# Optimization experiments

Hardware: AMD Instinct MI355X
Metric: run time of the kernel (lower is better)

## Reference

```python
import jax, jax.numpy as jnp
import numpy as np

N, E, F, H, R, NB, G, C = 100000, 500000, 128, 64, 16, 30, 1000, 10


def setup_inputs() -> dict:
    key = jax.random.key(0)
    ks = jax.random.split(key, 12)
    s = 0.05
    x = jax.random.normal(ks[0], (N, F), jnp.float32)
    edge_index = jax.random.randint(ks[1], (2, E), 0, N, dtype=jnp.int32)
    edge_norm = jax.random.uniform(ks[2], (E,), jnp.float32)
    edge_type = jax.random.randint(ks[3], (E,), 0, R, dtype=jnp.int32)
    seq_lengths = jnp.full((G,), N // G, dtype=jnp.int32)  # 1000 graphs x 100 nodes
    return dict(
        x=x, edge_index=edge_index, edge_norm=edge_norm, edge_type=edge_type,
        seq_lengths=seq_lengths, avec=0,
        w1_rel=jax.random.normal(ks[4], (F, H), jnp.float32) * s,
        w1_root=jax.random.normal(ks[5], (F, H), jnp.float32) * s,
        b1=jnp.zeros((H,), jnp.float32),
        bases=jax.random.normal(ks[6], (NB, H, H), jnp.float32) * s,
        comp=jax.random.normal(ks[7], (R, NB), jnp.float32) * s,
        w2_root=jax.random.normal(ks[8], (H, H), jnp.float32) * s,
        b2=jnp.zeros((H,), jnp.float32),
        lin_w=jax.random.normal(ks[9], (2 * (F + H), H), jnp.float32) * s,
        lin_b=jnp.zeros((H,), jnp.float32),
        fc_w=jax.random.normal(ks[10], (H, C), jnp.float32) * s,
        fc_b=jnp.zeros((C,), jnp.float32),
    )


def reference(x, edge_index, edge_norm, edge_type, seq_lengths, avec,
              w1_rel, w1_root, b1, bases, comp, w2_root, b2,
              lin_w, lin_b, fc_w, fc_b):
    src, dst = edge_index[0], edge_index[1]

    # --- GraphConv (PyG): out_i = W_rel @ sum_{j->i} w_ji x_j + W_root x_i + b
    msg = x[src] * edge_norm[:, None]                       # [E, F]
    agg = jax.ops.segment_sum(msg, dst, num_segments=N)     # [N, F]
    h = agg @ w1_rel + x @ w1_root + b1                     # [N, H]

    # --- RGCNConv with basis decomposition, mean aggregation per relation
    W = jnp.einsum('rb,bio->rio', comp, bases)              # [R, H, H]
    hs = h[src]                                             # [E, H]
    out = h @ w2_root + b2                                  # root transform + bias
    for r in range(R):  # small fixed relation count
        m = (edge_type == r).astype(h.dtype)                # [E]
        s_r = jax.ops.segment_sum(hs * m[:, None], dst, num_segments=N)
        c_r = jax.ops.segment_sum(m, dst, num_segments=N)
        out = out + (s_r / jnp.maximum(c_r, 1.0)[:, None]) @ W[r]

    feats = jnp.concatenate([x, out], axis=-1)              # [N, F+H]

    # --- ragged per-graph sum & max pooling (replaces the Python loop)
    bounds = jnp.cumsum(seq_lengths)
    gid = jnp.searchsorted(bounds, jnp.arange(N), side='right')  # [N] graph ids
    gsum = jax.ops.segment_sum(feats, gid, num_segments=G)       # [G, F+H]
    gmax = jax.ops.segment_max(feats, gid, num_segments=G)       # [G, F+H]

    hidden = jax.nn.relu(jnp.concatenate([gsum, gmax], -1) @ lin_w + lin_b)
    # dropout is identity at inference
    logits = hidden @ fc_w + fc_b                           # [G, C]
    if avec:
        return logits
    return jax.nn.log_softmax(logits, -1)
```

## Files before the change

### kernel.cpp

```cpp
#include <hip/hip_runtime.h>
#include <hip/hip_bf16.h>

#define NN 100000
#define NE 500000
#define FD 128
#define HD 64
#define RR 16
#define NBASE 30
#define GG 1000
#define CC 10
#define NGROUP 6250
#define NBLK ((NE + 255) / 256)
#define NDBLK ((NN + 256) / 256)
#define NOBLK (NN / 16)
#define NPBLK ((NGROUP + 3) / 4)
#define TOTZ (NN * RR)
#define ZBLK ((TOTZ + 1023) / 1024)


typedef __attribute__((ext_vector_type(8))) short bf16x8;
typedef __attribute__((ext_vector_type(4))) float f32x4;

__device__ inline unsigned short f2b(float x) {
  __hip_bfloat16 b = __float2bfloat16(x);
  return *reinterpret_cast<unsigned short*>(&b);
}
__device__ inline float b2f(unsigned short u) {
  return __uint_as_float(((unsigned)u) << 16);
}
__device__ inline unsigned pk2(float a, float b) {
  return (unsigned)f2b(a) | ((unsigned)f2b(b) << 16);
}

__device__ inline int block_scan_incl(int v, int* ps, int t) {
  ps[t] = v;
  __syncthreads();
  for (int off = 1; off < 256; off <<= 1) {
    int u = (t >= off) ? ps[t - off] : 0;
    __syncthreads();
    ps[t] += u;
    __syncthreads();
  }
  return ps[t];
}

__global__ void k_prep(const float* comp, const float* bases, const float* w_root,
                       const float* w_rel, const float* w2, const int* seq,
                       unsigned short* Wt, unsigned short* wcat2, unsigned short* w2t,
                       int* zbase, int* bounds) {
  int bx = blockIdx.x;
  if (bx < 256) {
    int idx = bx * 256 + threadIdx.x;
    int r = idx >> 12, kj = idx & 4095;
    int k = kj >> 6, n = kj & 63;
    float acc = 0.0f;
    for (int b = 0; b < NBASE; ++b)
      acc += comp[r * NBASE + b] * bases[b * 4096 + kj];
    int sk = (k & 15) * 4 + (k >> 4);
    Wt[(r << 12) + n * 64 + sk] = f2b(acc);
  } else if (bx < 336) {
    int idx = (bx - 256) * 256 + threadIdx.x;
    if (idx < 16384) {
      int n = idx >> 7, k = idx & 127;
      float v = (n < 64) ? w_root[k * 64 + n] : w_rel[k * 64 + (n - 64)];
      int nt = n >> 4, m = n & 15;
      int s = k >> 5, q = (k >> 3) & 3, j = k & 7;
      wcat2[(((nt * 4 + s) * 64) + q * 16 + m) * 8 + j] = f2b(v);
    } else if (idx < 16384 + 4096) {
      int i2 = idx - 16384;
      int n = i2 >> 6, k = i2 & 63;
      int sk = (k & 15) * 4 + (k >> 4);
      w2t[n * 64 + sk] = f2b(w2[k * 64 + n]);
    }
  } else if (bx == 336) {
    __shared__ int ps[256];
    int t = threadIdx.x;
    int loc[4];
    int ss = 0;
    if (t < 250) {
      for (int i = 0; i < 4; ++i) { loc[i] = seq[t * 4 + i]; ss += loc[i]; }
    }
    int incl = block_scan_incl(ss, ps, t);
    int base = incl - ss;
    if (t < 250) {
      int run = base;
      for (int i = 0; i < 4; ++i) { run += loc[i]; bounds[t * 4 + i] = run; }
    }
  } else {
    int idx = (bx - 337) * 1024 + threadIdx.x * 4;
    if (idx < TOTZ)
      *reinterpret_cast<int4*>(zbase + idx) = make_int4(0, 0, 0, 0);
  }
}

__global__ __launch_bounds__(256) void k_projhists(
    const float* x, const unsigned short* wcat2, const float* b1,
    unsigned short* hroot_bf, unsigned short* xw_bf,
    const int* ei, const int* etype, int* bch, int* hist2) {
  __shared__ unsigned short wsh[16384];
  __shared__ int lh[RR];
  if (blockIdx.x < NBLK) {
    if (threadIdx.x < RR) lh[threadIdx.x] = 0;
    __syncthreads();
    int e = blockIdx.x * 256 + threadIdx.x;
    if (e < NE) {
      int t = etype[e];
      atomicAdd(&lh[t], 1);
      atomicAdd(&hist2[ei[NE + e] * RR + t], 1);
    }
    __syncthreads();
    if (threadIdx.x < RR) bch[blockIdx.x * RR + threadIdx.x] = lh[threadIdx.x];
    return;
  }
  int bx = blockIdx.x - NBLK;
  int wv = threadIdx.x >> 6, l = threadIdx.x & 63, m = l & 15, q = l >> 4;
  int g = bx * 4 + wv;
  bool active = (g < NGROUP);
  int gc = active ? g : (NGROUP - 1);
  size_t n0 = (size_t)gc * 16;
  const float* xr = x + (n0 + m) * FD + q * 8;
  float4 xv[8];
#pragma unroll
  for (int s = 0; s < 4; ++s) {
    xv[2 * s] = *reinterpret_cast<const float4*>(xr + s * 32);
    xv[2 * s + 1] = *reinterpret_cast<const float4*>(xr + s * 32 + 4);
  }
  {
    const uint4* wsrc = reinterpret_cast<const uint4*>(wcat2);
    uint4* wdst = reinterpret_cast<uint4*>(wsh);
#pragma unroll
    for (int r = 0; r < 8; ++r)
      wdst[r * 256 + threadIdx.x] = wsrc[r * 256 + threadIdx.x];
  }
  __syncthreads();
  if (!active) return;
  bf16x8 afr[4];
#pragma unroll
  for (int s = 0; s < 4; ++s) {
    float4 xa = xv[2 * s], xb = xv[2 * s + 1];
    bf16x8 a;
    a[0] = (short)f2b(xa.x); a[1] = (short)f2b(xa.y);
    a[2] = (short)f2b(xa.z); a[3] = (short)f2b(xa.w);
    a[4] = (short)f2b(xb.x); a[5] = (short)f2b(xb.y);
    a[6] = (short)f2b(xb.z); a[7] = (short)f2b(xb.w);
    afr[s] = a;
  }
  f32x4 acc[8];
#pragma unroll
  for (int nt = 0; nt < 8; ++nt) acc[nt] = (f32x4){0, 0, 0, 0};
#pragma unroll
  for (int s = 0; s < 4; ++s) {
#pragma unroll
    for (int nt = 0; nt < 8; ++nt) {
      bf16x8 b = *reinterpret_cast<const bf16x8*>(wsh + (size_t)((nt * 4 + s) * 64 + l) * 8);
      acc[nt] = __builtin_amdgcn_mfma_f32_16x16x32_bf16(afr[s], b, acc[nt], 0, 0, 0);
    }
  }
  float bv[4];
#pragma unroll
  for (int nt = 0; nt < 4; ++nt) bv[nt] = b1[nt * 16 + m];
#pragma unroll
  for (int i = 0; i < 4; ++i) {
    size_t row = (n0 + q * 4 + i) * 64 + m * 4;
    uint2 oh, ox;
    oh.x = pk2(acc[0][i] + bv[0], acc[1][i] + bv[1]);
    oh.y = pk2(acc[2][i] + bv[2], acc[3][i] + bv[3]);
    ox.x = pk2(acc[4][i], acc[5][i]);
    ox.y = pk2(acc[6][i], acc[7][i]);
    *reinterpret_cast<uint2*>(hroot_bf + row) = oh;
    *reinterpret_cast<uint2*>(xw_bf + row) = ox;
  }
}

__device__ inline int dst_degree(const int* hist2, int dst) {
  const int4* hp = reinterpret_cast<const int4*>(hist2 + dst * RR);
  int4 a = hp[0], b = hp[1], c = hp[2], d = hp[3];
  return a.x + a.y + a.z + a.w + b.x + b.y + b.z + b.w +
         c.x + c.y + c.z + c.w + d.x + d.y + d.z + d.w;
}

__global__ void k_scanA(const int* hist2, int* bsum) {
  __shared__ int red[256];
  int t = threadIdx.x;
  int dst = blockIdx.x * 256 + t;
  red[t] = (dst < NN) ? dst_degree(hist2, dst) : 0;
  __syncthreads();
  for (int s = 128; s; s >>= 1) {
    if (t < s) red[t] += red[t + s];
    __syncthreads();
  }
  if (t == 0) bsum[blockIdx.x] = red[0];
}

__global__ void k_scanC(const int* hist2, const int* bsum, int* rowptr_d, int* ctr_d) {
  int t = threadIdx.x;
  int dst = blockIdx.x * 256 + t;
  int v = (dst < NN) ? dst_degree(hist2, dst) : 0;
  __shared__ int ps[256];
  int incl = block_scan_incl(v, ps, t);
  int ex = bsum[blockIdx.x] + incl - v;
  if (dst <= NN) { rowptr_d[dst] = ex; ctr_d[dst] = ex; }
}

__global__ void k_bscan(const int* bch, int* bsum, int* bbase, int* offs) {
  __shared__ int part[16][17], chunkbase[16][17];
  __shared__ int colbase[16];
  __shared__ int ps[256];
  int t = threadIdx.x;
  {
    int i0 = t * 2, i1 = t * 2 + 1;
    int l0 = (i0 < NDBLK) ? bsum[i0] : 0;
    int l1 = (i1 < NDBLK) ? bsum[i1] : 0;
    int sa = l0 + l1;
    int incla = block_scan_incl(sa, ps, t);
    int run = incla - sa;
    if (i0 < NDBLK) bsum[i0] = run;
    run += l0;
    if (i1 < NDBLK) bsum[i1] = run;
  }
  __syncthreads();
  int ty = t & 15, ck = t >> 4;
  const int CH = (NBLK + 15) / 16;
  int b0 = ck * CH, b1 = min(b0 + CH, NBLK);
  int s = 0;
  for (int b = b0; b < b1; ++b) s += bch[b * 16 + ty];
  part[ck][ty] = s;
  __syncthreads();
  if (t < 16) {
    int run = 0;
    for (int c = 0; c < 16; ++c) { chunkbase[c][t] = run; run += part[c][t]; }
    colbase[t] = run;
  }
  __syncthreads();
  if (t == 0) {
    int run = 0;
    for (int r = 0; r < RR; ++r) { int v = colbase[r]; offs[r] = run; colbase[r] = run; run += v; }
    offs[RR] = run;
  }
  __syncthreads();
  {
    int run = colbase[ty] + chunkbase[ck][ty];
    for (int b = b0; b < b1; ++b) {
      int v = bch[b * 16 + ty];
      bbase[b * 16 + ty] = run;
      run += v;
    }
  }
}

__global__ void k_sort(const int* ei, const int* etype, const float* enorm,
                       const int* bbase, const int* hist2, int* ctr_d,
                       uint4* tse, uint2* esen) {
  __shared__ int lcnt[RR];
  if (threadIdx.x < RR) lcnt[threadIdx.x] = 0;
  __syncthreads();
  int e = blockIdx.x * 256 + threadIdx.x;
  if (e >= NE) return;
  int t = etype[e];
  int rank = atomicAdd(&lcnt[t], 1);
  int p = bbase[blockIdx.x * RR + t] + rank;
  int src = ei[e];
  int dst = ei[NE + e];
  int cnt = hist2[dst * RR + t];
  float inv = 1.0f / (float)max(cnt, 1);
  int pos = atomicAdd(&ctr_d[dst], 1);
  esen[pos] = make_uint2((unsigned)src, __float_as_uint(enorm[e]));
  tse[p] = make_uint4((unsigned)src, __float_as_uint(inv), (unsigned)pos, 0u);
}

__global__ __launch_bounds__(256) void k_gconv_seg(const int* rowptr_d, const uint2* esen,
    const unsigned short* xw_bf, const unsigned short* hroot_bf, unsigned short* h_bf) {
  int wv = threadIdx.x >> 6, l = threadIdx.x & 63;
  int c4 = l & 15, eq = l >> 4;
  int dst = blockIdx.x * 4 + wv;
  int lo = rowptr_d[dst];
  int hi = rowptr_d[dst + 1];
  float4 acc = {0.0f, 0.0f, 0.0f, 0.0f};
  for (int base0 = lo; base0 < hi; base0 += 64) {
    int n = min(64, hi - base0);
    int sv = 0;
    float nv = 0.0f;
    if (l < n) {
      uint2 se = esen[base0 + l];
      sv = (int)se.x;
      nv = __uint_as_float(se.y);
    }
    int k4max = (n + 3) >> 2;
    for (int k4 = 0; k4 < k4max; ++k4) {
      int eid = k4 * 4 + eq;
      int s = __shfl(sv, eid);
      float w = __shfl(nv, eid);
      if (eid < n) {
        uint2 v = *reinterpret_cast<const uint2*>(xw_bf + (size_t)s * 64 + c4 * 4);
        acc.x += b2f((unsigned short)(v.x & 0xffffu)) * w;
        acc.y += b2f((unsigned short)(v.x >> 16)) * w;
        acc.z += b2f((unsigned short)(v.y & 0xffffu)) * w;
        acc.w += b2f((unsigned short)(v.y >> 16)) * w;
      }
    }
  }
  acc.x += __shfl_xor(acc.x, 16); acc.y += __shfl_xor(acc.y, 16);
  acc.z += __shfl_xor(acc.z, 16); acc.w += __shfl_xor(acc.w, 16);
  acc.x += __shfl_xor(acc.x, 32); acc.y += __shfl_xor(acc.y, 32);
  acc.z += __shfl_xor(acc.z, 32); acc.w += __shfl_xor(acc.w, 32);
  if (l < 16) {
    uint2 hb = *reinterpret_cast<const uint2*>(hroot_bf + (size_t)dst * 64 + l * 4);
    acc.x += b2f((unsigned short)(hb.x & 0xffffu));
    acc.y += b2f((unsigned short)(hb.x >> 16));
    acc.z += b2f((unsigned short)(hb.y & 0xffffu));
    acc.w += b2f((unsigned short)(hb.y >> 16));
    uint2 o;
    o.x = pk2(acc.x, acc.y);
    o.y = pk2(acc.z, acc.w);
    *reinterpret_cast<uint2*>(h_bf + (size_t)dst * 64 + l * 4) = o;
  }
}

__global__ __launch_bounds__(256) void k_rgcn_y(const uint4* tse, const int* offs,
    const unsigned short* h_bf, const unsigned short* Wt, unsigned short* y_bf) {
  int r = blockIdx.x;
  int lo = offs[r], hi = offs[r + 1];
  int cnt = hi - lo;
  int wv = threadIdx.x >> 6;
  int l = threadIdx.x & 63;
  int m = l & 15, q = l >> 4;
  int ngroups = (cnt + 15) / 16;
  const unsigned short* Wr = Wt + (r << 12);
  bf16x8 bfr[2][4];
#pragma unroll
  for (int s = 0; s < 2; ++s)
#pragma unroll
    for (int nt = 0; nt < 4; ++nt)
      bfr[s][nt] = *reinterpret_cast<const bf16x8*>(Wr + (nt * 16 + m) * 64 + s * 32 + q * 8);

  for (int g = blockIdx.y * 4 + wv; g < ngroups; g += gridDim.y * 4) {
    int base = lo + g * 16;
    int ne = min(16, hi - base);
    int p = base + ((m < ne) ? m : 0);
    uint4 t4 = tse[p];
    int src = (int)t4.x;
    float inv = __uint_as_float(t4.y);
    int pos = (int)t4.z;
    f32x4 acc[4];
#pragma unroll
    for (int nt = 0; nt < 4; ++nt) acc[nt] = (f32x4){0, 0, 0, 0};
    const unsigned short* hrow = h_bf + (size_t)src * 64 + q * 8;
#pragma unroll
    for (int s = 0; s < 2; ++s) {
      bf16x8 afr = *reinterpret_cast<const bf16x8*>(hrow + s * 32);
#pragma unroll
      for (int nt = 0; nt < 4; ++nt)
        acc[nt] = __builtin_amdgcn_mfma_f32_16x16x32_bf16(afr, bfr[s][nt], acc[nt], 0, 0, 0);
    }
#pragma unroll
    for (int i = 0; i < 4; ++i) {
      int row = q * 4 + i;
      float ir = __shfl(inv, row);
      int pr = __shfl(pos, row);
      if (row < ne) {
        uint2 o;
        o.x = pk2(acc[0][i] * ir, acc[1][i] * ir);
        o.y = pk2(acc[2][i] * ir, acc[3][i] * ir);
        *reinterpret_cast<uint2*>(y_bf + (size_t)pr * 64 + m * 4) = o;
      }
    }
  }
}

__global__ __launch_bounds__(256) void k_out(const int* rowptr_d, const unsigned short* y_bf,
    const unsigned short* h_bf, const unsigned short* w2t, const float* b2,
    const int* bounds, float* psum_p, float* pmax_p) {
  __shared__ float ldsC[16][68];
  __shared__ int gidv[16];
  int wv = threadIdx.x >> 6, l = threadIdx.x & 63;
  int c4 = l & 15, eq = l >> 4;
  size_t d0 = (size_t)blockIdx.x * 16;
  if (threadIdx.x < 16) {
    int dst = (int)d0 + threadIdx.x;
    int lo2 = 0, hi2 = GG;
    while (lo2 < hi2) {
      int mid = (lo2 + hi2) >> 1;
      if (bounds[mid] <= dst) lo2 = mid + 1; else hi2 = mid;
    }
    gidv[threadIdx.x] = lo2;
  }
  for (int dd = 0; dd < 4; ++dd) {
    int dst = (int)d0 + wv * 4 + dd;
    int lo = rowptr_d[dst];
    int hi = rowptr_d[dst + 1];
    float4 acc = {0.0f, 0.0f, 0.0f, 0.0f};
    for (int row = lo + eq; row < hi; row += 4) {
      uint2 v = *reinterpret_cast<const uint2*>(y_bf + (size_t)row * 64 + c4 * 4);
      acc.x += b2f((unsigned short)(v.x & 0xffffu));
      acc.y += b2f((unsigned short)(v.x >> 16));
      acc.z += b2f((unsigned short)(v.y & 0xffffu));
      acc.w += b2f((unsigned short)(v.y >> 16));
    }
    acc.x += __shfl_xor(acc.x, 16); acc.y += __shfl_xor(acc.y, 16);
    acc.z += __shfl_xor(acc.z, 16); acc.w += __shfl_xor(acc.w, 16);
    acc.x += __shfl_xor(acc.x, 32); acc.y += __shfl_xor(acc.y, 32);
    acc.z += __shfl_xor(acc.z, 32); acc.w += __shfl_xor(acc.w, 32);
    if (l < 16)
      *reinterpret_cast<float4*>(&ldsC[wv * 4 + dd][l * 4]) = acc;
  }
  __syncthreads();
  int m = l & 15, q = l >> 4, nt = wv;
  float bb = b2[nt * 16 + m];
  f32x4 acc;
#pragma unroll
  for (int i = 0; i < 4; ++i) acc[i] = ldsC[q * 4 + i][m * 4 + nt] + bb;
#pragma unroll
  for (int s = 0; s < 2; ++s) {
    bf16x8 a = *reinterpret_cast<const bf16x8*>(h_bf + (d0 + m) * 64 + s * 32 + q * 8);
    bf16x8 b = *reinterpret_cast<const bf16x8*>(w2t + (nt * 16 + m) * 64 + s * 32 + q * 8);
    acc = __builtin_amdgcn_mfma_f32_16x16x32_bf16(a, b, acc, 0, 0, 0);
  }
  int c = nt * 16 + m;
  int gA = gidv[0];
  float sA = 0.0f, xA = -3.4e38f, sB = 0.0f, xB = -3.4e38f;
#pragma unroll
  for (int i = 0; i < 4; ++i) {
    int gi = gidv[q * 4 + i];
    if (gi == gA) { sA += acc[i]; xA = fmaxf(xA, acc[i]); }
    else          { sB += acc[i]; xB = fmaxf(xB, acc[i]); }
  }
#pragma unroll
  for (int off = 16; off <= 32; off <<= 1) {
    sA += __shfl_xor(sA, off); xA = fmaxf(xA, __shfl_xor(xA, off));
    sB += __shfl_xor(sB, off); xB = fmaxf(xB, __shfl_xor(xB, off));
  }
  if (q == 0) {
    size_t base = (size_t)blockIdx.x * 128;
    psum_p[base + c] = sA;
    psum_p[base + 64 + c] = sB;
    pmax_p[base + c] = xA;
    pmax_p[base + 64 + c] = xB;
  }
}

__global__ __launch_bounds__(256) void k_head(const float* x, const int* bounds,
    const float* psum_p, const float* pmax_p, const float* lin_w, const float* lin_b,
    const float* fc_w, const float* fc_b, float* dout) {
  __shared__ float4 psum[8][32], pmax[8][32];
  __shared__ float gsum[192], gmax[192];
  __shared__ float part[4][64];
  __shared__ float hid[HD], lg[CC], mred[2];
  int g = blockIdx.x, t = threadIdx.x;
  int lo = (g == 0) ? 0 : bounds[g - 1];
  int hi = bounds[g];
  int nn = hi - lo;
  {
    int c4 = t & 31, ch = t >> 5;
    int a = lo + (nn * ch) / 8, b = lo + (nn * (ch + 1)) / 8;
    float4 s = {0, 0, 0, 0};
    float4 mx = {-3.4e38f, -3.4e38f, -3.4e38f, -3.4e38f};
    const float* bp = x + (size_t)a * FD + c4 * 4;
    int n = a;
    for (; n + 4 <= b; n += 4) {
      float4 v0 = *reinterpret_cast<const float4*>(bp);
      float4 v1 = *reinterpret_cast<const float4*>(bp + FD);
      float4 v2 = *reinterpret_cast<const float4*>(bp + 2 * FD);
      float4 v3 = *reinterpret_cast<const float4*>(bp + 3 * FD);
      bp += 4 * FD;
      s.x += v0.x + v1.x + v2.x + v3.x;
      s.y += v0.y + v1.y + v2.y + v3.y;
      s.z += v0.z + v1.z + v2.z + v3.z;
      s.w += v0.w + v1.w + v2.w + v3.w;
      mx.x = fmaxf(fmaxf(fmaxf(mx.x, v0.x), fmaxf(v1.x, v2.x)), v3.x);
      mx.y = fmaxf(fmaxf(fmaxf(mx.y, v0.y), fmaxf(v1.y, v2.y)), v3.y);
      mx.z = fmaxf(fmaxf(fmaxf(mx.z, v0.z), fmaxf(v1.z, v2.z)), v3.z);
      mx.w = fmaxf(fmaxf(fmaxf(mx.w, v0.w), fmaxf(v1.w, v2.w)), v3.w);
    }
    for (; n < b; ++n) {
      float4 v = *reinterpret_cast<const float4*>(bp);
      bp += FD;
      s.x += v.x; s.y += v.y; s.z += v.z; s.w += v.w;
      mx.x = fmaxf(mx.x, v.x); mx.y = fmaxf(mx.y, v.y);
      mx.z = fmaxf(mx.z, v.z); mx.w = fmaxf(mx.w, v.w);
    }
    psum[ch][c4] = s;
    pmax[ch][c4] = mx;
  }
  __syncthreads();
  if (t < 32) {
    float4 s = psum[0][t], m = pmax[0][t];
#pragma unroll
    for (int ch = 1; ch < 8; ++ch) {
      float4 ps = psum[ch][t], pm = pmax[ch][t];
      s.x += ps.x; s.y += ps.y; s.z += ps.z; s.w += ps.w;
      m.x = fmaxf(m.x, pm.x); m.y = fmaxf(m.y, pm.y);
      m.z = fmaxf(m.z, pm.z); m.w = fmaxf(m.w, pm.w);
    }
    gsum[t * 4 + 0] = s.x; gsum[t * 4 + 1] = s.y;
    gsum[t * 4 + 2] = s.z; gsum[t * 4 + 3] = s.w;
    gmax[t * 4 + 0] = m.x; gmax[t * 4 + 1] = m.y;
    gmax[t * 4 + 2] = m.z; gmax[t * 4 + 3] = m.w;
  } else if (t < 96) {
    int c = t - 32;
    int blo = lo >> 4, bhi = (hi - 1) >> 4;
    float s = 0.0f, mx = -3.4e38f;
    for (int b = blo; b <= bhi; ++b) {
      size_t base = (size_t)b * 128;
      if (b * 16 >= lo) {
        s += psum_p[base + c];
        mx = fmaxf(mx, pmax_p[base + c]);
      }
      if (b * 16 + 15 < hi) {
        s += psum_p[base + 64 + c];
        mx = fmaxf(mx, pmax_p[base + 64 + c]);
      }
    }
    gsum[128 + c] = s;
    gmax[128 + c] = mx;
  }
  __syncthreads();
  {
    int o = t & 63, pp = t >> 6;
    float a = 0.0f;
    int k0 = pp * 96;
    for (int k = k0; k < k0 + 96; ++k) {
      float gv = (k < 192) ? gsum[k] : gmax[k - 192];
      a += gv * lin_w[k * 64 + o];
    }
    part[pp][o] = a;
  }
  __syncthreads();
  if (t < HD) {
    float a = lin_b[t] + part[0][t] + part[1][t] + part[2][t] + part[3][t];
    hid[t] = fmaxf(a, 0.0f);
  }
  __syncthreads();
  if (t < CC) {
    float a = fc_b[t];
    for (int k = 0; k < HD; ++k) a += hid[k] * fc_w[k * CC + t];
    lg[t] = a;
  }
  __syncthreads();
  if (t == 0) {
    float mm = lg[0];
#pragma unroll
    for (int i = 1; i < CC; ++i) mm = fmaxf(mm, lg[i]);
    float se = 0.0f;
#pragma unroll
    for (int i = 0; i < CC; ++i) se += __expf(lg[i] - mm);
    mred[0] = mm;
    mred[1] = __logf(se);
  }
  __syncthreads();
  if (t < CC) dout[g * CC + t] = lg[t] - mred[0] - mred[1];
}

extern "C" void kernel_launch(void* const* d_in, const int* in_sizes, int n_in,
                              void* d_out, int out_size, void* d_ws, size_t ws_size,
                              hipStream_t stream) {
  const float* x     = (const float*)d_in[0];
  const int* ei      = (const int*)d_in[1];
  const float* enorm = (const float*)d_in[2];
  const int* etype   = (const int*)d_in[3];
  const int* seq     = (const int*)d_in[4];
  const float* w1_rel  = (const float*)d_in[6];
  const float* w1_root = (const float*)d_in[7];
  const float* b1      = (const float*)d_in[8];
  const float* bases   = (const float*)d_in[9];
  const float* comp    = (const float*)d_in[10];
  const float* w2      = (const float*)d_in[11];
  const float* b2      = (const float*)d_in[12];
  const float* lin_w   = (const float*)d_in[13];
  const float* lin_b   = (const float*)d_in[14];
  const float* fc_w    = (const float*)d_in[15];
  const float* fc_b    = (const float*)d_in[16];
  float* dout = (float*)d_out;

  char* p = (char*)d_ws;
  unsigned short* hroot_bf = (unsigned short*)p; p += (size_t)NN * 64 * 2;
  unsigned short* xw_bf    = (unsigned short*)p; p += (size_t)NN * 64 * 2;
  unsigned short* y_bf = (unsigned short*)p; p += (size_t)NE * 64 * 2;
  unsigned short* h_bf = (unsigned short*)p; p += (size_t)NN * 64 * 2;
  unsigned short* Wt   = (unsigned short*)p; p += (size_t)RR * 4096 * 2;
  unsigned short* wcat2 = (unsigned short*)p; p += (size_t)128 * 128 * 2;
  unsigned short* w2t  = (unsigned short*)p; p += (size_t)64 * 64 * 2;
  uint4* tse   = (uint4*)p; p += (size_t)NE * 16;
  uint2* esen  = (uint2*)p; p += (size_t)NE * 8;
  int* hist2   = (int*)p; p += (size_t)NN * RR * 4;
  float* psum_p = (float*)p; p += (size_t)NOBLK * 128 * 4;
  float* pmax_p = (float*)p; p += (size_t)NOBLK * 128 * 4;
  int* rowptr_d = (int*)p; p += (size_t)(NDBLK * 256) * 4;
  int* ctr_d   = (int*)p; p += (size_t)(NDBLK * 256) * 4;
  int* bch     = (int*)p; p += (size_t)NBLK * RR * 4;
  int* bbase   = (int*)p; p += (size_t)NBLK * RR * 4;
  int* bsum    = (int*)p; p += (size_t)NGROUP * 4;
  int* offs    = (int*)p; p += 68;
  int* bounds  = (int*)p; p += (size_t)GG * 4;

  hipLaunchKernelGGL(k_prep, dim3(337 + ZBLK), dim3(256), 0, stream,
                     comp, bases, w1_root, w1_rel, w2, seq, Wt, wcat2, w2t, hist2, bounds);
  hipLaunchKernelGGL(k_projhists, dim3(NBLK + NPBLK), dim3(256), 0, stream,
                     x, wcat2, b1, hroot_bf, xw_bf, ei, etype, bch, hist2);
  hipLaunchKernelGGL(k_scanA, dim3(NDBLK), dim3(256), 0, stream, hist2, bsum);
  hipLaunchKernelGGL(k_bscan, dim3(1), dim3(256), 0, stream, bch, bsum, bbase, offs);
  hipLaunchKernelGGL(k_scanC, dim3(NDBLK), dim3(256), 0, stream, hist2, bsum, rowptr_d, ctr_d);
  hipLaunchKernelGGL(k_sort, dim3(NBLK), dim3(256), 0, stream,
                     ei, etype, enorm, bbase, hist2, ctr_d, tse, esen);
  hipLaunchKernelGGL(k_gconv_seg, dim3(NN / 4), dim3(256), 0, stream,
                     rowptr_d, esen, xw_bf, hroot_bf, h_bf);
  hipLaunchKernelGGL(k_rgcn_y, dim3(RR, 128), dim3(256), 0, stream,
                     tse, offs, h_bf, Wt, y_bf);
  hipLaunchKernelGGL(k_out, dim3(NOBLK), dim3(256), 0, stream,
                     rowptr_d, y_bf, h_bf, w2t, b2, bounds, psum_p, pmax_p);
  hipLaunchKernelGGL(k_head, dim3(GG), dim3(256), 0, stream, x, bounds,
                     psum_p, pmax_p, lin_w, lin_b, fc_w, fc_b, dout);
}
```

Before: 331.2 us.

## Aggregate per-relation means before weight transform, dropping edge-level RGCN matmul

Replaces the per-edge transform (h[src]·W_r written to a 500k×64 y buffer, then summed per destination) with per-destination, per-relation mean aggregation in LDS, followed by MFMA against the 16 relation weights. The relation-sorted edge list, its block scan and the tse buffer go away. Edge type is packed into the high bits of the source index in esen. This removes the large y_bf write and read, but adds LDS float atomics, a 64KB LDS buffer per block that limits occupancy, and 16 relation MFMAs per node tile. The packing assumes node ids fit in 20 bits.

Measured after the change: 560.8 us. +69.3%, slower.

```diff
diff --git a/kernel.cpp b/kernel.cpp
--- a/kernel.cpp
+++ b/kernel.cpp
@@ -96,20 +96,12 @@
 __global__ __launch_bounds__(256) void k_projhists(
     const float* x, const unsigned short* wcat2, const float* b1,
     unsigned short* hroot_bf, unsigned short* xw_bf,
-    const int* ei, const int* etype, int* bch, int* hist2) {
+    const int* ei, const int* etype, int* hist2) {
   __shared__ unsigned short wsh[16384];
-  __shared__ int lh[RR];
   if (blockIdx.x < NBLK) {
-    if (threadIdx.x < RR) lh[threadIdx.x] = 0;
-    __syncthreads();
     int e = blockIdx.x * 256 + threadIdx.x;
-    if (e < NE) {
-      int t = etype[e];
-      atomicAdd(&lh[t], 1);
-      atomicAdd(&hist2[ei[NE + e] * RR + t], 1);
-    }
-    __syncthreads();
-    if (threadIdx.x < RR) bch[blockIdx.x * RR + threadIdx.x] = lh[threadIdx.x];
+    if (e < NE)
+      atomicAdd(&hist2[ei[NE + e] * RR + etype[e]], 1);
     return;
   }
   int bx = blockIdx.x - NBLK;
@@ -192,6 +184,20 @@
   if (t == 0) bsum[blockIdx.x] = red[0];
 }
 
+__global__ void k_bsum(int* bsum) {
+  __shared__ int ps[256];
+  int t = threadIdx.x;
+  int i0 = t * 2, i1 = t * 2 + 1;
+  int l0 = (i0 < NDBLK) ? bsum[i0] : 0;
+  int l1 = (i1 < NDBLK) ? bsum[i1] : 0;
+  int sa = l0 + l1;
+  int incla = block_scan_incl(sa, ps, t);
+  int run = incla - sa;
+  if (i0 < NDBLK) bsum[i0] = run;
+  run += l0;
+  if (i1 < NDBLK) bsum[i1] = run;
+}
+
 __global__ void k_scanC(const int* hist2, const int* bsum, int* rowptr_d, int* ctr_d) {
   int t = threadIdx.x;
   int dst = blockIdx.x * 256 + t;
@@ -202,70 +208,15 @@
   if (dst <= NN) { rowptr_d[dst] = ex; ctr_d[dst] = ex; }
 }
 
-__global__ void k_bscan(const int* bch, int* bsum, int* bbase, int* offs) {
-  __shared__ int part[16][17], chunkbase[16][17];
-  __shared__ int colbase[16];
-  __shared__ int ps[256];
-  int t = threadIdx.x;
-  {
-    int i0 = t * 2, i1 = t * 2 + 1;
-    int l0 = (i0 < NDBLK) ? bsum[i0] : 0;
-    int l1 = (i1 < NDBLK) ? bsum[i1] : 0;
-    int sa = l0 + l1;
-    int incla = block_scan_incl(sa, ps, t);
-    int run = incla - sa;
-    if (i0 < NDBLK) bsum[i0] = run;
-    run += l0;
-    if (i1 < NDBLK) bsum[i1] = run;
-  }
-  __syncthreads();
-  int ty = t & 15, ck = t >> 4;
-  const int CH = (NBLK + 15) / 16;
-  int b0 = ck * CH, b1 = min(b0 + CH, NBLK);
-  int s = 0;
-  for (int b = b0; b < b1; ++b) s += bch[b * 16 + ty];
-  part[ck][ty] = s;
-  __syncthreads();
-  if (t < 16) {
-    int run = 0;
-    for (int c = 0; c < 16; ++c) { chunkbase[c][t] = run; run += part[c][t]; }
-    colbase[t] = run;
-  }
-  __syncthreads();
-  if (t == 0) {
-    int run = 0;
-    for (int r = 0; r < RR; ++r) { int v = colbase[r]; offs[r] = run; colbase[r] = run; run += v; }
-    offs[RR] = run;
-  }
-  __syncthreads();
-  {
-    int run = colbase[ty] + chunkbase[ck][ty];
-    for (int b = b0; b < b1; ++b) {
-      int v = bch[b * 16 + ty];
-      bbase[b * 16 + ty] = run;
-      run += v;
-    }
-  }
-}
-
 __global__ void k_sort(const int* ei, const int* etype, const float* enorm,
-                       const int* bbase, const int* hist2, int* ctr_d,
-                       uint4* tse, uint2* esen) {
-  __shared__ int lcnt[RR];
-  if (threadIdx.x < RR) lcnt[threadIdx.x] = 0;
-  __syncthreads();
+                       int* ctr_d, uint2* esen) {
   int e = blockIdx.x * 256 + threadIdx.x;
   if (e >= NE) return;
   int t = etype[e];
-  int rank = atomicAdd(&lcnt[t], 1);
-  int p = bbase[blockIdx.x * RR + t] + rank;
   int src = ei[e];
   int dst = ei[NE + e];
-  int cnt = hist2[dst * RR + t];
-  float inv = 1.0f / (float)max(cnt, 1);
   int pos = atomicAdd(&ctr_d[dst], 1);
-  esen[pos] = make_uint2((unsigned)src, __float_as_uint(enorm[e]));
-  tse[p] = make_uint4((unsigned)src, __float_as_uint(inv), (unsigned)pos, 0u);
+  esen[pos] = make_uint2((unsigned)src | ((unsigned)t << 20), __float_as_uint(enorm[e]));
 }
 
 __global__ __launch_bounds__(256) void k_gconv_seg(const int* rowptr_d, const uint2* esen,
@@ -282,7 +233,7 @@
     float nv = 0.0f;
     if (l < n) {
       uint2 se = esen[base0 + l];
-      sv = (int)se.x;
+      sv = (int)(se.x & 0xFFFFFu);
       nv = __uint_as_float(se.y);
     }
     int k4max = (n + 3) >> 2;
@@ -316,113 +267,98 @@
   }
 }
 
-__global__ __launch_bounds__(256) void k_rgcn_y(const uint4* tse, const int* offs,
-    const unsigned short* h_bf, const unsigned short* Wt, unsigned short* y_bf) {
-  int r = blockIdx.x;
-  int lo = offs[r], hi = offs[r + 1];
-  int cnt = hi - lo;
-  int wv = threadIdx.x >> 6;
-  int l = threadIdx.x & 63;
-  int m = l & 15, q = l >> 4;
-  int ngroups = (cnt + 15) / 16;
-  const unsigned short* Wr = Wt + (r << 12);
-  bf16x8 bfr[2][4];
-#pragma unroll
-  for (int s = 0; s < 2; ++s)
-#pragma unroll
-    for (int nt = 0; nt < 4; ++nt)
-      bfr[s][nt] = *reinterpret_cast<const bf16x8*>(Wr + (nt * 16 + m) * 64 + s * 32 + q * 8);
-
-  for (int g = blockIdx.y * 4 + wv; g < ngroups; g += gridDim.y * 4) {
-    int base = lo + g * 16;
-    int ne = min(16, hi - base);
-    int p = base + ((m < ne) ? m : 0);
-    uint4 t4 = tse[p];
-    int src = (int)t4.x;
-    float inv = __uint_as_float(t4.y);
-    int pos = (int)t4.z;
-    f32x4 acc[4];
-#pragma unroll
-    for (int nt = 0; nt < 4; ++nt) acc[nt] = (f32x4){0, 0, 0, 0};
-    const unsigned short* hrow = h_bf + (size_t)src * 64 + q * 8;
-#pragma unroll
-    for (int s = 0; s < 2; ++s) {
-      bf16x8 afr = *reinterpret_cast<const bf16x8*>(hrow + s * 32);
-#pragma unroll
-      for (int nt = 0; nt < 4; ++nt)
-        acc[nt] = __builtin_amdgcn_mfma_f32_16x16x32_bf16(afr, bfr[s][nt], acc[nt], 0, 0, 0);
-    }
-#pragma unroll
-    for (int i = 0; i < 4; ++i) {
-      int row = q * 4 + i;
-      float ir = __shfl(inv, row);
-      int pr = __shfl(pos, row);
-      if (row < ne) {
-        uint2 o;
-        o.x = pk2(acc[0][i] * ir, acc[1][i] * ir);
-        o.y = pk2(acc[2][i] * ir, acc[3][i] * ir);
-        *reinterpret_cast<uint2*>(y_bf + (size_t)pr * 64 + m * 4) = o;
-      }
-    }
-  }
-}
-
-__global__ __launch_bounds__(256) void k_out(const int* rowptr_d, const unsigned short* y_bf,
-    const unsigned short* h_bf, const unsigned short* w2t, const float* b2,
-    const int* bounds, float* psum_p, float* pmax_p) {
-  __shared__ float ldsC[16][68];
-  __shared__ int gidv[16];
+__global__ __launch_bounds__(256) void k_out(const int* rowptr_d, const uint2* esen,
+    const int* hist2, const unsigned short* h_bf, const unsigned short* Wt,
+    const unsigned short* w2t, const float* b2, const int* bounds,
+    float* psum_p, float* pmax_p) {
+  __shared__ float s_lds[16 * 16 * 64];
   int wv = threadIdx.x >> 6, l = threadIdx.x & 63;
   int c4 = l & 15, eq = l >> 4;
   size_t d0 = (size_t)blockIdx.x * 16;
-  if (threadIdx.x < 16) {
-    int dst = (int)d0 + threadIdx.x;
-    int lo2 = 0, hi2 = GG;
-    while (lo2 < hi2) {
-      int mid = (lo2 + hi2) >> 1;
-      if (bounds[mid] <= dst) lo2 = mid + 1; else hi2 = mid;
-    }
-    gidv[threadIdx.x] = lo2;
-  }
-  for (int dd = 0; dd < 4; ++dd) {
-    int dst = (int)d0 + wv * 4 + dd;
-    int lo = rowptr_d[dst];
-    int hi = rowptr_d[dst + 1];
-    float4 acc = {0.0f, 0.0f, 0.0f, 0.0f};
-    for (int row = lo + eq; row < hi; row += 4) {
-      uint2 v = *reinterpret_cast<const uint2*>(y_bf + (size_t)row * 64 + c4 * 4);
-      acc.x += b2f((unsigned short)(v.x & 0xffffu));
-      acc.y += b2f((unsigned short)(v.x >> 16));
-      acc.z += b2f((unsigned short)(v.y & 0xffffu));
-      acc.w += b2f((unsigned short)(v.y >> 16));
-    }
-    acc.x += __shfl_xor(acc.x, 16); acc.y += __shfl_xor(acc.y, 16);
-    acc.z += __shfl_xor(acc.z, 16); acc.w += __shfl_xor(acc.w, 16);
-    acc.x += __shfl_xor(acc.x, 32); acc.y += __shfl_xor(acc.y, 32);
-    acc.z += __shfl_xor(acc.z, 32); acc.w += __shfl_xor(acc.w, 32);
-    if (l < 16)
-      *reinterpret_cast<float4*>(&ldsC[wv * 4 + dd][l * 4]) = acc;
+  {
+    float4* sz = reinterpret_cast<float4*>(s_lds);
+#pragma unroll
+    for (int i = 0; i < 16; ++i)
+      sz[i * 256 + threadIdx.x] = make_float4(0.0f, 0.0f, 0.0f, 0.0f);
+  }
+  __syncthreads();
+  for (int dd4 = 0; dd4 < 4; ++dd4) {
+    int dd = wv * 4 + dd4;
+    int dst = (int)d0 + dd;
+    int lo = rowptr_d[dst], hi = rowptr_d[dst + 1];
+    int swz = (dd & 7) << 3;
+    for (int base0 = lo; base0 < hi; base0 += 64) {
+      int n = min(64, hi - base0);
+      int sv = 0, tv = 0;
+      float iv = 0.0f;
+      if (l < n) {
+        uint2 se = esen[base0 + l];
+        sv = (int)(se.x & 0xFFFFFu);
+        tv = (int)(se.x >> 20);
+        iv = 1.0f / (float)max(hist2[dst * RR + tv], 1);
+      }
+      int k4max = (n + 3) >> 2;
+      for (int k4 = 0; k4 < k4max; ++k4) {
+        int eid = k4 * 4 + eq;
+        int s = __shfl(sv, eid);
+        int ty = __shfl(tv, eid);
+        float w = __shfl(iv, eid);
+        if (eid < n) {
+          uint2 v = *reinterpret_cast<const uint2*>(h_bf + (size_t)s * 64 + c4 * 4);
+          float* sp = s_lds + (dd * 16 + ty) * 64 + ((c4 * 4) ^ swz);
+          atomicAdd(sp + 0, b2f((unsigned short)(v.x & 0xffffu)) * w);
+          atomicAdd(sp + 1, b2f((unsigned short)(v.x >> 16)) * w);
+          atomicAdd(sp + 2, b2f((unsigned short)(v.y & 0xffffu)) * w);
+          atomicAdd(sp + 3, b2f((unsigned short)(v.y >> 16)) * w);
+        }
+      }
+    }
   }
   __syncthreads();
   int m = l & 15, q = l >> 4, nt = wv;
-  float bb = b2[nt * 16 + m];
-  f32x4 acc;
-#pragma unroll
-  for (int i = 0; i < 4; ++i) acc[i] = ldsC[q * 4 + i][m * 4 + nt] + bb;
+  f32x4 acc = (f32x4){0.0f, 0.0f, 0.0f, 0.0f};
+  {
+    int swz = (m & 7) << 3;
+    for (int r = 0; r < RR; ++r) {
+      const unsigned short* Wr = Wt + (r << 12) + (nt * 16 + m) * 64 + q * 8;
+      const float* arow = s_lds + (m * 16 + r) * 64;
+#pragma unroll
+      for (int s = 0; s < 2; ++s) {
+        const float* ap = arow + ((s * 32 + q * 8) ^ swz);
+        bf16x8 a;
+#pragma unroll
+        for (int j = 0; j < 8; ++j) a[j] = (short)f2b(ap[j]);
+        bf16x8 b = *reinterpret_cast<const bf16x8*>(Wr + s * 32);
+        acc = __builtin_amdgcn_mfma_f32_16x16x32_bf16(a, b, acc, 0, 0, 0);
+      }
+    }
+  }
 #pragma unroll
   for (int s = 0; s < 2; ++s) {
     bf16x8 a = *reinterpret_cast<const bf16x8*>(h_bf + (d0 + m) * 64 + s * 32 + q * 8);
     bf16x8 b = *reinterpret_cast<const bf16x8*>(w2t + (nt * 16 + m) * 64 + s * 32 + q * 8);
     acc = __builtin_amdgcn_mfma_f32_16x16x32_bf16(a, b, acc, 0, 0, 0);
   }
+  float bb = b2[nt * 16 + m];
+#pragma unroll
+  for (int i = 0; i < 4; ++i) acc[i] += bb;
   int c = nt * 16 + m;
-  int gA = gidv[0];
+  int gA;
+  {
+    int lo2 = 0, hi2 = GG;
+    while (lo2 < hi2) {
+      int mid = (lo2 + hi2) >> 1;
+      if (bounds[mid] <= (int)d0) lo2 = mid + 1; else hi2 = mid;
+    }
+    gA = lo2;
+  }
+  int bndA = bounds[gA];
   float sA = 0.0f, xA = -3.4e38f, sB = 0.0f, xB = -3.4e38f;
 #pragma unroll
   for (int i = 0; i < 4; ++i) {
-    int gi = gidv[q * 4 + i];
-    if (gi == gA) { sA += acc[i]; xA = fmaxf(xA, acc[i]); }
-    else          { sB += acc[i]; xB = fmaxf(xB, acc[i]); }
+    int row = (int)d0 + q * 4 + i;
+    if (row < bndA) { sA += acc[i]; xA = fmaxf(xA, acc[i]); }
+    else            { sB += acc[i]; xB = fmaxf(xB, acc[i]); }
   }
 #pragma unroll
   for (int off = 16; off <= 32; off <<= 1) {
@@ -574,39 +510,32 @@
   char* p = (char*)d_ws;
   unsigned short* hroot_bf = (unsigned short*)p; p += (size_t)NN * 64 * 2;
   unsigned short* xw_bf    = (unsigned short*)p; p += (size_t)NN * 64 * 2;
-  unsigned short* y_bf = (unsigned short*)p; p += (size_t)NE * 64 * 2;
   unsigned short* h_bf = (unsigned short*)p; p += (size_t)NN * 64 * 2;
   unsigned short* Wt   = (unsigned short*)p; p += (size_t)RR * 4096 * 2;
   unsigned short* wcat2 = (unsigned short*)p; p += (size_t)128 * 128 * 2;
   unsigned short* w2t  = (unsigned short*)p; p += (size_t)64 * 64 * 2;
-  uint4* tse   = (uint4*)p; p += (size_t)NE * 16;
   uint2* esen  = (uint2*)p; p += (size_t)NE * 8;
   int* hist2   = (int*)p; p += (size_t)NN * RR * 4;
   float* psum_p = (float*)p; p += (size_t)NOBLK * 128 * 4;
   float* pmax_p = (float*)p; p += (size_t)NOBLK * 128 * 4;
   int* rowptr_d = (int*)p; p += (size_t)(NDBLK * 256) * 4;
   int* ctr_d   = (int*)p; p += (size_t)(NDBLK * 256) * 4;
-  int* bch     = (int*)p; p += (size_t)NBLK * RR * 4;
-  int* bbase   = (int*)p; p += (size_t)NBLK * RR * 4;
   int* bsum    = (int*)p; p += (size_t)NGROUP * 4;
-  int* offs    = (int*)p; p += 68;
   int* bounds  = (int*)p; p += (size_t)GG * 4;
 
   hipLaunchKernelGGL(k_prep, dim3(337 + ZBLK), dim3(256), 0, stream,
                      comp, bases, w1_root, w1_rel, w2, seq, Wt, wcat2, w2t, hist2, bounds);
   hipLaunchKernelGGL(k_projhists, dim3(NBLK + NPBLK), dim3(256), 0, stream,
-                     x, wcat2, b1, hroot_bf, xw_bf, ei, etype, bch, hist2);
+                     x, wcat2, b1, hroot_bf, xw_bf, ei, etype, hist2);
   hipLaunchKernelGGL(k_scanA, dim3(NDBLK), dim3(256), 0, stream, hist2, bsum);
-  hipLaunchKernelGGL(k_bscan, dim3(1), dim3(256), 0, stream, bch, bsum, bbase, offs);
+  hipLaunchKernelGGL(k_bsum, dim3(1), dim3(256), 0, stream, bsum);
   hipLaunchKernelGGL(k_scanC, dim3(NDBLK), dim3(256), 0, stream, hist2, bsum, rowptr_d, ctr_d);
   hipLaunchKernelGGL(k_sort, dim3(NBLK), dim3(256), 0, stream,
-                     ei, etype, enorm, bbase, hist2, ctr_d, tse, esen);
+                     ei, etype, enorm, ctr_d, esen);
   hipLaunchKernelGGL(k_gconv_seg, dim3(NN / 4), dim3(256), 0, stream,
                      rowptr_d, esen, xw_bf, hroot_bf, h_bf);
-  hipLaunchKernelGGL(k_rgcn_y, dim3(RR, 128), dim3(256), 0, stream,
-                     tse, offs, h_bf, Wt, y_bf);
   hipLaunchKernelGGL(k_out, dim3(NOBLK), dim3(256), 0, stream,
-                     rowptr_d, y_bf, h_bf, w2t, b2, bounds, psum_p, pmax_p);
+                     rowptr_d, esen, hist2, h_bf, Wt, w2t, b2, bounds, psum_p, pmax_p);
   hipLaunchKernelGGL(k_head, dim3(GG), dim3(256), 0, stream, x, bounds,
                      psum_p, pmax_p, lin_w, lin_b, fc_w, fc_b, dout);
 }
```
